# Performance work log

Hardware: AMD Instinct MI355X
Metric: run time of the kernel (lower is better)

Reference implementation:

```python
import jax, jax.numpy as jnp
import numpy as np


def log_g(x):
    # log of the 'continuous' g: g(x) = x + 0.5 for x>=0, sigmoid(x) otherwise
    return jnp.where(x >= 0, jnp.log(jax.nn.relu(x) + 0.5), -jax.nn.softplus(-x))


def setup_inputs() -> dict:
    key = jax.random.key(0)
    ks = jax.random.split(key, 6)
    B, T, D, H = 8, 4096, 1024, 1024
    s = 1.0 / np.sqrt(D)
    return {
        "x": jax.random.normal(ks[0], (B, T, D), dtype=jnp.float32),
        "h_0": jax.random.uniform(ks[1], (B, 1, H), dtype=jnp.float32),
        "Wz": jax.random.normal(ks[2], (D, H), dtype=jnp.float32) * s,
        "bz": jnp.zeros((H,), dtype=jnp.float32),
        "Wh": jax.random.normal(ks[3], (D, H), dtype=jnp.float32) * s,
        "bh": jnp.zeros((H,), dtype=jnp.float32),
    }


def reference(x, h_0, Wz, bz, Wh, bh):
    # x: [B,T,D], h_0: [B,1,H]
    k = jnp.einsum('btd,dh->bth', x, Wz) + bz            # gate pre-activation
    log_z = -jax.nn.softplus(-k)                          # log sigmoid(k)
    log_coeffs = -jax.nn.softplus(k)                      # log (1 - sigmoid(k))
    log_h0 = log_g(h_0)                                   # [B,1,H]
    log_tilde_h = log_g(jnp.einsum('btd,dh->bth', x, Wh) + bh)
    # parallel scan in log space over time axis
    a_star = jnp.pad(jnp.cumsum(log_coeffs, axis=1), ((0, 0), (1, 0), (0, 0)))  # [B,T+1,H]
    log_values = jnp.concatenate([log_h0, log_z + log_tilde_h], axis=1)          # [B,T+1,H]
    log_h = a_star + jax.lax.cumlogsumexp(log_values - a_star, axis=1)
    return jnp.exp(log_h)  # [B,T+1,H]
```

## Files before the change

### kernel.cpp

```cpp
#include <hip/hip_runtime.h>
#include <hip/hip_bf16.h>
#include <cstdint>
#include <cstddef>

#define B_ 8
#define T_ 4096
#define D_ 1024
#define H_ 1024
#define M_ (B_*T_)
#define NCHUNK 64
#define CLEN 64

using bf16x8   = __attribute__((ext_vector_type(8))) __bf16;
using floatx4  = __attribute__((ext_vector_type(4))) float;
using float4v  = __attribute__((ext_vector_type(4))) float;
using ushort4v = __attribute__((ext_vector_type(4))) unsigned short;
using aw2_t    = __attribute__((ext_vector_type(2))) _Float16;
using halfx8   = __attribute__((ext_vector_type(8))) _Float16;

__device__ inline unsigned short f2bf(float f) {
  union { float f; unsigned u; } v; v.f = f;
  unsigned u = v.u;
  u += 0x7fffu + ((u >> 16) & 1u);
  return (unsigned short)(u >> 16);
}

__device__ inline void async_load16(const void* g, void* l) {
  __builtin_amdgcn_global_load_lds((const __attribute__((address_space(1))) void*)g,
                                   (__attribute__((address_space(3))) void*)l,
                                   16, 0, 0);
}

__global__ __launch_bounds__(256) void cast_x_kernel(const float* __restrict__ x,
                                                     unsigned short* __restrict__ xb) {
  size_t i = ((size_t)blockIdx.x * 256 + threadIdx.x) * 2;
#pragma unroll
  for (int j = 0; j < 2; ++j) {
    float4v v = ((const float4v*)x)[i + j];
    ushort4v o = { f2bf(v[0]), f2bf(v[1]), f2bf(v[2]), f2bf(v[3]) };
    ((ushort4v*)xb)[i + j] = o;
  }
}

__global__ __launch_bounds__(256) void transpose_w_kernel(const float* __restrict__ Wz,
                                                          const float* __restrict__ Wh,
                                                          unsigned short* __restrict__ Wzt,
                                                          unsigned short* __restrict__ Wht) {
  __shared__ float tile[32][33];
  const float* W = blockIdx.z ? Wh : Wz;
  unsigned short* Wt = blockIdx.z ? Wht : Wzt;
  int n0 = blockIdx.x * 32, k0 = blockIdx.y * 32;
#pragma unroll
  for (int j = 0; j < 4; ++j) {
    int kr = threadIdx.y + j * 8;
    tile[kr][threadIdx.x] = W[(size_t)(k0 + kr) * H_ + n0 + threadIdx.x];
  }
  __syncthreads();
#pragma unroll
  for (int j = 0; j < 4; ++j) {
    int nr = threadIdx.y + j * 8;
    Wt[(size_t)(n0 + nr) * D_ + k0 + threadIdx.x] = f2bf(tile[threadIdx.x][nr]);
  }
}

__global__ __launch_bounds__(256, 2) void gemm_kernel(
    const unsigned short* __restrict__ xb,
    const unsigned short* __restrict__ wzt,
    const unsigned short* __restrict__ wht,
    const float* __restrict__ bz, const float* __restrict__ bh,
    aw2_t* __restrict__ aw_out) {
  __shared__ __align__(16) unsigned short ldsA[128 * 64];
  __shared__ __align__(16) unsigned short ldsBz[128 * 64];
  __shared__ __align__(16) unsigned short ldsBh[128 * 64];

  const int tid = threadIdx.x;
  const int lane = tid & 63, wid = tid >> 6;
  const int wm = wid >> 1, wn = wid & 1;
  const int row16 = lane & 15, quad = lane >> 4;

  int g = blockIdx.x;
  int x = g & 7, j = g >> 3;
  int n_idx = j & 7;
  int m_idx = (x << 5) | (j >> 3);
  const int m0 = m_idx * 128, n0 = n_idx * 128;

  floatx4 accz[4][4], acch[4][4];
#pragma unroll
  for (int mi = 0; mi < 4; ++mi)
#pragma unroll
    for (int ni = 0; ni < 4; ++ni) {
      accz[mi][ni] = (floatx4){0.f, 0.f, 0.f, 0.f};
      acch[mi][ni] = (floatx4){0.f, 0.f, 0.f, 0.f};
    }

  const int srow = tid >> 3;
  const int jblk = ((tid & 7) - srow) & 7;
  const unsigned short* aSrc  = xb  + (size_t)(m0 + srow) * D_ + jblk * 8;
  const unsigned short* zSrc  = wzt + (size_t)(n0 + srow) * D_ + jblk * 8;
  const unsigned short* hSrc  = wht + (size_t)(n0 + srow) * D_ + jblk * 8;

  const int p0 = (quad + row16) & 7;
  const int p1 = p0 ^ 4;

  for (int kk = 0; kk < D_; kk += 64) {
#pragma unroll
    for (int t = 0; t < 4; ++t) {
      size_t roff = (size_t)(32 * t) * D_ + kk;
      int doff = (tid + 256 * t) * 8;
      async_load16(aSrc + roff, &ldsA[doff]);
      async_load16(zSrc + roff, &ldsBz[doff]);
      async_load16(hSrc + roff, &ldsBh[doff]);
    }
    __syncthreads();

#pragma unroll
    for (int kh = 0; kh < 2; ++kh) {
      const int p = kh ? p1 : p0;
      bf16x8 af[4], bzf[4], bhf[4];
#pragma unroll
      for (int mi = 0; mi < 4; ++mi)
        af[mi] = *(const bf16x8*)&ldsA[(wm * 64 + mi * 16 + row16) * 64 + p * 8];
#pragma unroll
      for (int ni = 0; ni < 4; ++ni) {
        bzf[ni] = *(const bf16x8*)&ldsBz[(wn * 64 + ni * 16 + row16) * 64 + p * 8];
        bhf[ni] = *(const bf16x8*)&ldsBh[(wn * 64 + ni * 16 + row16) * 64 + p * 8];
      }
#pragma unroll
      for (int mi = 0; mi < 4; ++mi)
#pragma unroll
        for (int ni = 0; ni < 4; ++ni) {
          accz[mi][ni] = __builtin_amdgcn_mfma_f32_16x16x32_bf16(af[mi], bzf[ni], accz[mi][ni], 0, 0, 0);
          acch[mi][ni] = __builtin_amdgcn_mfma_f32_16x16x32_bf16(af[mi], bhf[ni], acch[mi][ni], 0, 0, 0);
        }
    }
    __syncthreads();
  }

#pragma unroll
  for (int mi = 0; mi < 4; ++mi) {
#pragma unroll
    for (int ni = 0; ni < 4; ++ni) {
      int col = n0 + wn * 64 + ni * 16 + row16;
      float bzv = bz[col], bhv = bh[col];
#pragma unroll
      for (int r = 0; r < 4; ++r) {
        int row = m0 + wm * 64 + mi * 16 + quad * 4 + r;
        float k   = accz[mi][ni][r] + bzv;
        float pre = acch[mi][ni][r] + bhv;
        float z  = 1.f / (1.f + __expf(-k));
        float av = 1.f / (1.f + __expf(k));
        float gg = (pre >= 0.f) ? (pre + 0.5f) : 1.f / (1.f + __expf(-pre));
        aw2_t o = { (_Float16)av, (_Float16)(z * gg) };
        aw_out[(size_t)row * H_ + col] = o;
      }
    }
  }
}

__global__ __launch_bounds__(256) void scan_pass1(const halfx8* __restrict__ aw,
                                                  float* __restrict__ P, float* __restrict__ S) {
  int c = blockIdx.x;
  int b = blockIdx.y;
  int h4 = threadIdx.x;
  size_t base = (size_t)(b * T_ + c * CLEN) * (H_ / 4) + h4;
  float p0 = 1.f, p1 = 1.f, p2 = 1.f, p3 = 1.f;
  float s0 = 0.f, s1 = 0.f, s2 = 0.f, s3 = 0.f;
#pragma unroll 8
  for (int i = 0; i < CLEN; ++i) {
    halfx8 v = aw[base + (size_t)i * (H_ / 4)];
    float a0 = (float)v[0], w0 = (float)v[1];
    float a1 = (float)v[2], w1 = (float)v[3];
    float a2 = (float)v[4], w2 = (float)v[5];
    float a3 = (float)v[6], w3 = (float)v[7];
    s0 = a0 * s0 + w0; p0 *= a0;
    s1 = a1 * s1 + w1; p1 *= a1;
    s2 = a2 * s2 + w2; p2 *= a2;
    s3 = a3 * s3 + w3; p3 *= a3;
  }
  size_t o = ((size_t)b * H_ + h4 * 4) * NCHUNK + c;
  P[o] = p0; P[o + NCHUNK] = p1; P[o + 2 * NCHUNK] = p2; P[o + 3 * NCHUNK] = p3;
  S[o] = s0; S[o + NCHUNK] = s1; S[o + 2 * NCHUNK] = s2; S[o + 3 * NCHUNK] = s3;
}

__global__ __launch_bounds__(256) void scan_pass2(const float* __restrict__ h0,
                                                  const float* __restrict__ P,
                                                  const float* __restrict__ S,
                                                  float* __restrict__ carry,
                                                  float* __restrict__ out) {
  int gid = blockIdx.x * 256 + threadIdx.x;
  int b = gid >> 10, h = gid & 1023;
  float v = h0[(size_t)b * H_ + h];
  float cur = (v >= 0.f) ? (v + 0.5f) : 1.f / (1.f + __expf(-v));
  out[((size_t)b * (T_ + 1)) * H_ + h] = cur;
  const float4v* Pv = (const float4v*)&P[((size_t)b * H_ + h) * NCHUNK];
  const float4v* Sv = (const float4v*)&S[((size_t)b * H_ + h) * NCHUNK];
  float4v* Cv = (float4v*)&carry[((size_t)b * H_ + h) * NCHUNK];
#pragma unroll
  for (int j = 0; j < NCHUNK / 4; ++j) {
    float4v p = Pv[j], s = Sv[j], cc;
    cc[0] = cur; cur = p[0] * cur + s[0];
    cc[1] = cur; cur = p[1] * cur + s[1];
    cc[2] = cur; cur = p[2] * cur + s[2];
    cc[3] = cur; cur = p[3] * cur + s[3];
    Cv[j] = cc;
  }
}

__global__ __launch_bounds__(256) void scan_pass3(const halfx8* __restrict__ aw,
                                                  const float* __restrict__ carry,
                                                  float* __restrict__ out) {
  int c = blockIdx.x;
  int b = blockIdx.y;
  int h4 = threadIdx.x;
  size_t base = (size_t)(b * T_ + c * CLEN) * (H_ / 4) + h4;
  size_t cb = ((size_t)b * H_ + h4 * 4) * NCHUNK + c;
  float c0 = carry[cb], c1 = carry[cb + NCHUNK], c2 = carry[cb + 2 * NCHUNK], c3 = carry[cb + 3 * NCHUNK];
  size_t obase = ((size_t)b * (T_ + 1) + c * CLEN + 1) * (H_ / 4) + h4;
  float4v* outv = (float4v*)out;
#pragma unroll 8
  for (int i = 0; i < CLEN; ++i) {
    halfx8 v = aw[base + (size_t)i * (H_ / 4)];
    c0 = (float)v[0] * c0 + (float)v[1];
    c1 = (float)v[2] * c1 + (float)v[3];
    c2 = (float)v[4] * c2 + (float)v[5];
    c3 = (float)v[6] * c3 + (float)v[7];
    float4v o = { c0, c1, c2, c3 };
    outv[obase + (size_t)i * (H_ / 4)] = o;
  }
}

extern "C" void kernel_launch(void* const* d_in, const int* in_sizes, int n_in,
                              void* d_out, int out_size, void* d_ws, size_t ws_size,
                              hipStream_t stream) {
  const float* x  = (const float*)d_in[0];
  const float* h0 = (const float*)d_in[1];
  const float* Wz = (const float*)d_in[2];
  const float* bz = (const float*)d_in[3];
  const float* Wh = (const float*)d_in[4];
  const float* bh = (const float*)d_in[5];
  float* out = (float*)d_out;

  char* ws = (char*)d_ws;
  unsigned short* xb  = (unsigned short*)(ws);
  unsigned short* wzt = (unsigned short*)(ws + 67108864ULL);
  unsigned short* wht = (unsigned short*)(ws + 69206016ULL);
  aw2_t* aw_ws = (aw2_t*)(ws + 71303168ULL);
  float* P_ws  = (float*)(ws + 71303168ULL + 134217728ULL);
  float* S_ws  = (float*)(ws + 71303168ULL + 134217728ULL + 2097152ULL);
  float* c_ws  = (float*)(ws + 71303168ULL + 134217728ULL + 2ULL * 2097152ULL);

  hipLaunchKernelGGL(cast_x_kernel, dim3(16384), dim3(256), 0, stream, x, xb);
  hipLaunchKernelGGL(transpose_w_kernel, dim3(32, 32, 2), dim3(32, 8), 0, stream, Wz, Wh, wzt, wht);
  hipLaunchKernelGGL(gemm_kernel, dim3(2048), dim3(256), 0, stream,
                     xb, wzt, wht, bz, bh, aw_ws);
  hipLaunchKernelGGL(scan_pass1, dim3(NCHUNK, B_), dim3(256), 0, stream,
                     (const halfx8*)aw_ws, P_ws, S_ws);
  hipLaunchKernelGGL(scan_pass2, dim3(32), dim3(256), 0, stream, h0, P_ws, S_ws, c_ws, out);
  hipLaunchKernelGGL(scan_pass3, dim3(NCHUNK, B_), dim3(256), 0, stream,
                     (const halfx8*)aw_ws, c_ws, out);
}
```

Baseline: 475.9 us.

## Restructure fused GEMM into 512-thread 256x128 tiles with 4-stage async pipeline

```diff
diff --git a/kernel.cpp b/kernel.cpp
--- a/kernel.cpp
+++ b/kernel.cpp
@@ -63,15 +63,15 @@
   }
 }
 
-__global__ __launch_bounds__(256, 2) void gemm_kernel(
+__global__ __launch_bounds__(512, 2) void gemm_kernel(
     const unsigned short* __restrict__ xb,
     const unsigned short* __restrict__ wzt,
     const unsigned short* __restrict__ wht,
     const float* __restrict__ bz, const float* __restrict__ bh,
     aw2_t* __restrict__ aw_out) {
-  __shared__ __align__(16) unsigned short ldsA[128 * 64];
-  __shared__ __align__(16) unsigned short ldsBz[128 * 64];
-  __shared__ __align__(16) unsigned short ldsBh[128 * 64];
+  __shared__ __align__(16) unsigned short ldsA[4][8192];
+  __shared__ __align__(16) unsigned short ldsBz[4][4096];
+  __shared__ __align__(16) unsigned short ldsBh[4][4096];
 
   const int tid = threadIdx.x;
   const int lane = tid & 63, wid = tid >> 6;
@@ -81,8 +81,8 @@
   int g = blockIdx.x;
   int x = g & 7, j = g >> 3;
   int n_idx = j & 7;
-  int m_idx = (x << 5) | (j >> 3);
-  const int m0 = m_idx * 128, n0 = n_idx * 128;
+  int m_idx = (x << 4) | (j >> 3);
+  const int m0 = m_idx << 8, n0 = n_idx << 7;
 
   floatx4 accz[4][4], acch[4][4];
 #pragma unroll
@@ -93,48 +93,105 @@
       acch[mi][ni] = (floatx4){0.f, 0.f, 0.f, 0.f};
     }
 
-  const int srow = tid >> 3;
-  const int jblk = ((tid & 7) - srow) & 7;
-  const unsigned short* aSrc  = xb  + (size_t)(m0 + srow) * D_ + jblk * 8;
-  const unsigned short* zSrc  = wzt + (size_t)(n0 + srow) * D_ + jblk * 8;
-  const unsigned short* hSrc  = wht + (size_t)(n0 + srow) * D_ + jblk * 8;
-
-  const int p0 = (quad + row16) & 7;
-  const int p1 = p0 ^ 4;
-
-  for (int kk = 0; kk < D_; kk += 64) {
-#pragma unroll
-    for (int t = 0; t < 4; ++t) {
-      size_t roff = (size_t)(32 * t) * D_ + kk;
-      int doff = (tid + 256 * t) * 8;
-      async_load16(aSrc + roff, &ldsA[doff]);
-      async_load16(zSrc + roff, &ldsBz[doff]);
-      async_load16(hSrc + roff, &ldsBh[doff]);
-    }
-    __syncthreads();
-
-#pragma unroll
-    for (int kh = 0; kh < 2; ++kh) {
-      const int p = kh ? p1 : p0;
-      bf16x8 af[4], bzf[4], bhf[4];
-#pragma unroll
-      for (int mi = 0; mi < 4; ++mi)
-        af[mi] = *(const bf16x8*)&ldsA[(wm * 64 + mi * 16 + row16) * 64 + p * 8];
-#pragma unroll
-      for (int ni = 0; ni < 4; ++ni) {
-        bzf[ni] = *(const bf16x8*)&ldsBz[(wn * 64 + ni * 16 + row16) * 64 + p * 8];
-        bhf[ni] = *(const bf16x8*)&ldsBh[(wn * 64 + ni * 16 + row16) * 64 + p * 8];
-      }
-#pragma unroll
-      for (int mi = 0; mi < 4; ++mi)
-#pragma unroll
-        for (int ni = 0; ni < 4; ++ni) {
-          accz[mi][ni] = __builtin_amdgcn_mfma_f32_16x16x32_bf16(af[mi], bzf[ni], accz[mi][ni], 0, 0, 0);
-          acch[mi][ni] = __builtin_amdgcn_mfma_f32_16x16x32_bf16(af[mi], bhf[ni], acch[mi][ni], 0, 0, 0);
-        }
-    }
-    __syncthreads();
-  }
+  const int srow = tid >> 2;
+  const int jA = ((tid & 3) - ((tid >> 3) & 3)) & 3;
+  const unsigned short* aS0 = xb  + (size_t)(m0 + srow) * D_ + jA * 8;
+  const unsigned short* aS1 = aS0 + (size_t)128 * D_;
+  const unsigned short* zS  = wzt + (size_t)(n0 + srow) * D_ + jA * 8;
+  const unsigned short* hS  = wht + (size_t)(n0 + srow) * D_ + jA * 8;
+
+  const int sl = (quad + (row16 >> 1)) & 3;
+  const int aoff = (wm * 64 + row16) * 32 + sl * 8;
+  const int boff = (wn * 64 + row16) * 32 + sl * 8;
+
+  async_load16(aS0 +  0, &ldsA[0][tid * 8]);
+  async_load16(aS1 +  0, &ldsA[0][tid * 8 + 4096]);
+  async_load16(zS  +  0, &ldsBz[0][tid * 8]);
+  async_load16(hS  +  0, &ldsBh[0][tid * 8]);
+  async_load16(aS0 + 32, &ldsA[1][tid * 8]);
+  async_load16(aS1 + 32, &ldsA[1][tid * 8 + 4096]);
+  async_load16(zS  + 32, &ldsBz[1][tid * 8]);
+  async_load16(hS  + 32, &ldsBh[1][tid * 8]);
+  asm volatile("s_waitcnt vmcnt(4)" ::: "memory");
+  __builtin_amdgcn_s_barrier();
+
+#define MFMA16(ACC, BF)                                                          \
+  __builtin_amdgcn_s_setprio(1);                                                 \
+  _Pragma("unroll")                                                              \
+  for (int mi = 0; mi < 4; ++mi)                                                 \
+    _Pragma("unroll")                                                            \
+    for (int ni = 0; ni < 4; ++ni)                                               \
+      ACC[mi][ni] = __builtin_amdgcn_mfma_f32_16x16x32_bf16(af[mi], BF[ni],      \
+                                                            ACC[mi][ni], 0, 0, 0); \
+  __builtin_amdgcn_s_setprio(0);
+
+#pragma unroll 1
+  for (int kt = 0; kt < 16; ++kt) {
+    const int s0 = (2 * kt) & 3, s1 = s0 + 1;
+    const int t0 = (s0 + 2) & 3, t1 = (s0 + 3) & 3;
+    const int kN = ((kt + 1) & 15) * 64;
+    const bool st = (kt < 15);
+    bf16x8 af[4], bzf[4], bhf[4];
+
+#pragma unroll
+    for (int mi = 0; mi < 4; ++mi)
+      af[mi] = *(const bf16x8*)&ldsA[s0][aoff + mi * 512];
+#pragma unroll
+    for (int ni = 0; ni < 4; ++ni)
+      bzf[ni] = *(const bf16x8*)&ldsBz[s0][boff + ni * 512];
+    if (st) {
+      async_load16(aS0 + kN, &ldsA[t0][tid * 8]);
+      async_load16(aS1 + kN, &ldsA[t0][tid * 8 + 4096]);
+    }
+    __builtin_amdgcn_s_barrier();
+    asm volatile("s_waitcnt lgkmcnt(0)" ::: "memory");
+    MFMA16(accz, bzf)
+    __builtin_amdgcn_s_barrier();
+
+#pragma unroll
+    for (int ni = 0; ni < 4; ++ni)
+      bhf[ni] = *(const bf16x8*)&ldsBh[s0][boff + ni * 512];
+    if (st) {
+      async_load16(zS + kN, &ldsBz[t0][tid * 8]);
+      async_load16(hS + kN, &ldsBh[t0][tid * 8]);
+      asm volatile("s_waitcnt vmcnt(4)" ::: "memory");
+    } else {
+      asm volatile("s_waitcnt vmcnt(0)" ::: "memory");
+    }
+    __builtin_amdgcn_s_barrier();
+    asm volatile("s_waitcnt lgkmcnt(0)" ::: "memory");
+    MFMA16(acch, bhf)
+    __builtin_amdgcn_s_barrier();
+
+#pragma unroll
+    for (int mi = 0; mi < 4; ++mi)
+      af[mi] = *(const bf16x8*)&ldsA[s1][aoff + mi * 512];
+#pragma unroll
+    for (int ni = 0; ni < 4; ++ni)
+      bzf[ni] = *(const bf16x8*)&ldsBz[s1][boff + ni * 512];
+    if (st) {
+      async_load16(aS0 + kN + 32, &ldsA[t1][tid * 8]);
+      async_load16(aS1 + kN + 32, &ldsA[t1][tid * 8 + 4096]);
+    }
+    __builtin_amdgcn_s_barrier();
+    asm volatile("s_waitcnt lgkmcnt(0)" ::: "memory");
+    MFMA16(accz, bzf)
+    __builtin_amdgcn_s_barrier();
+
+#pragma unroll
+    for (int ni = 0; ni < 4; ++ni)
+      bhf[ni] = *(const bf16x8*)&ldsBh[s1][boff + ni * 512];
+    if (st) {
+      async_load16(zS + kN + 32, &ldsBz[t1][tid * 8]);
+      async_load16(hS + kN + 32, &ldsBh[t1][tid * 8]);
+      asm volatile("s_waitcnt vmcnt(4)" ::: "memory");
+    }
+    __builtin_amdgcn_s_barrier();
+    asm volatile("s_waitcnt lgkmcnt(0)" ::: "memory");
+    MFMA16(acch, bhf)
+    __builtin_amdgcn_s_barrier();
+  }
+#undef MFMA16
 
 #pragma unroll
   for (int mi = 0; mi < 4; ++mi) {
@@ -251,7 +308,7 @@
 
   hipLaunchKernelGGL(cast_x_kernel, dim3(16384), dim3(256), 0, stream, x, xb);
   hipLaunchKernelGGL(transpose_w_kernel, dim3(32, 32, 2), dim3(32, 8), 0, stream, Wz, Wh, wzt, wht);
-  hipLaunchKernelGGL(gemm_kernel, dim3(2048), dim3(256), 0, stream,
+  hipLaunchKernelGGL(gemm_kernel, dim3(1024), dim3(512), 0, stream,
                      xb, wzt, wht, bz, bh, aw_ws);
   hipLaunchKernelGGL(scan_pass1, dim3(NCHUNK, B_), dim3(256), 0, stream,
                      (const halfx8*)aw_ws, P_ws, S_ws);
```

Measured after the change: 490.9 us. +3.2%, slower.

## Fuse three-pass chunked scan into single decoupled-lookback kernel and merge prep kernels

Applied to the files above, without the earlier changes.

```diff
diff --git a/kernel.cpp b/kernel.cpp
--- a/kernel.cpp
+++ b/kernel.cpp
@@ -31,35 +31,42 @@
                                    16, 0, 0);
 }
 
-__global__ __launch_bounds__(256) void cast_x_kernel(const float* __restrict__ x,
-                                                     unsigned short* __restrict__ xb) {
-  size_t i = ((size_t)blockIdx.x * 256 + threadIdx.x) * 2;
-#pragma unroll
-  for (int j = 0; j < 2; ++j) {
-    float4v v = ((const float4v*)x)[i + j];
-    ushort4v o = { f2bf(v[0]), f2bf(v[1]), f2bf(v[2]), f2bf(v[3]) };
-    ((ushort4v*)xb)[i + j] = o;
-  }
-}
-
-__global__ __launch_bounds__(256) void transpose_w_kernel(const float* __restrict__ Wz,
-                                                          const float* __restrict__ Wh,
-                                                          unsigned short* __restrict__ Wzt,
-                                                          unsigned short* __restrict__ Wht) {
+__global__ __launch_bounds__(256) void prep_kernel(const float* __restrict__ x,
+                                                   unsigned short* __restrict__ xb,
+                                                   const float* __restrict__ Wz,
+                                                   const float* __restrict__ Wh,
+                                                   unsigned short* __restrict__ Wzt,
+                                                   unsigned short* __restrict__ Wht) {
   __shared__ float tile[32][33];
-  const float* W = blockIdx.z ? Wh : Wz;
-  unsigned short* Wt = blockIdx.z ? Wht : Wzt;
-  int n0 = blockIdx.x * 32, k0 = blockIdx.y * 32;
-#pragma unroll
-  for (int j = 0; j < 4; ++j) {
-    int kr = threadIdx.y + j * 8;
-    tile[kr][threadIdx.x] = W[(size_t)(k0 + kr) * H_ + n0 + threadIdx.x];
-  }
-  __syncthreads();
-#pragma unroll
-  for (int j = 0; j < 4; ++j) {
-    int nr = threadIdx.y + j * 8;
-    Wt[(size_t)(n0 + nr) * D_ + k0 + threadIdx.x] = f2bf(tile[threadIdx.x][nr]);
+  const int bid = blockIdx.x;
+  if (bid < 16384) {
+    size_t i = ((size_t)bid * 256 + threadIdx.x) * 2;
+#pragma unroll
+    for (int j = 0; j < 2; ++j) {
+      float4v v = ((const float4v*)x)[i + j];
+      ushort4v o = { f2bf(v[0]), f2bf(v[1]), f2bf(v[2]), f2bf(v[3]) };
+      ((ushort4v*)xb)[i + j] = o;
+    }
+  } else {
+    const int b2 = bid - 16384;
+    const int z = b2 >> 10;
+    const int rem = b2 & 1023;
+    const int bx = rem & 31, by = rem >> 5;
+    const int tx = threadIdx.x & 31, ty = threadIdx.x >> 5;
+    const float* W = z ? Wh : Wz;
+    unsigned short* Wt = z ? Wht : Wzt;
+    const int n0 = bx * 32, k0 = by * 32;
+#pragma unroll
+    for (int j = 0; j < 4; ++j) {
+      int kr = ty + j * 8;
+      tile[kr][tx] = W[(size_t)(k0 + kr) * H_ + n0 + tx];
+    }
+    __syncthreads();
+#pragma unroll
+    for (int j = 0; j < 4; ++j) {
+      int nr = ty + j * 8;
+      Wt[(size_t)(n0 + nr) * D_ + k0 + tx] = f2bf(tile[tx][nr]);
+    }
   }
 }
 
@@ -157,12 +164,18 @@
   }
 }
 
-__global__ __launch_bounds__(256) void scan_pass1(const halfx8* __restrict__ aw,
-                                                  float* __restrict__ P, float* __restrict__ S) {
-  int c = blockIdx.x;
-  int b = blockIdx.y;
-  int h4 = threadIdx.x;
-  size_t base = (size_t)(b * T_ + c * CLEN) * (H_ / 4) + h4;
+__global__ __launch_bounds__(256) void scan_fused(const halfx8* __restrict__ aw,
+                                                  const float* __restrict__ h0,
+                                                  float4v* __restrict__ PL,
+                                                  float4v* __restrict__ SL,
+                                                  float4v* __restrict__ SI,
+                                                  int* __restrict__ flags,
+                                                  float* __restrict__ out) {
+  const int c = blockIdx.x & (NCHUNK - 1);
+  const int b = blockIdx.x >> 6;
+  const int h4 = threadIdx.x;
+  const size_t base = (size_t)(b * T_ + c * CLEN) * (H_ / 4) + h4;
+
   float p0 = 1.f, p1 = 1.f, p2 = 1.f, p3 = 1.f;
   float s0 = 0.f, s1 = 0.f, s2 = 0.f, s3 = 0.f;
 #pragma unroll 8
@@ -177,46 +190,65 @@
     s2 = a2 * s2 + w2; p2 *= a2;
     s3 = a3 * s3 + w3; p3 *= a3;
   }
-  size_t o = ((size_t)b * H_ + h4 * 4) * NCHUNK + c;
-  P[o] = p0; P[o + NCHUNK] = p1; P[o + 2 * NCHUNK] = p2; P[o + 3 * NCHUNK] = p3;
-  S[o] = s0; S[o + NCHUNK] = s1; S[o + 2 * NCHUNK] = s2; S[o + 3 * NCHUNK] = s3;
-}
-
-__global__ __launch_bounds__(256) void scan_pass2(const float* __restrict__ h0,
-                                                  const float* __restrict__ P,
-                                                  const float* __restrict__ S,
-                                                  float* __restrict__ carry,
-                                                  float* __restrict__ out) {
-  int gid = blockIdx.x * 256 + threadIdx.x;
-  int b = gid >> 10, h = gid & 1023;
-  float v = h0[(size_t)b * H_ + h];
-  float cur = (v >= 0.f) ? (v + 0.5f) : 1.f / (1.f + __expf(-v));
-  out[((size_t)b * (T_ + 1)) * H_ + h] = cur;
-  const float4v* Pv = (const float4v*)&P[((size_t)b * H_ + h) * NCHUNK];
-  const float4v* Sv = (const float4v*)&S[((size_t)b * H_ + h) * NCHUNK];
-  float4v* Cv = (float4v*)&carry[((size_t)b * H_ + h) * NCHUNK];
-#pragma unroll
-  for (int j = 0; j < NCHUNK / 4; ++j) {
-    float4v p = Pv[j], s = Sv[j], cc;
-    cc[0] = cur; cur = p[0] * cur + s[0];
-    cc[1] = cur; cur = p[1] * cur + s[1];
-    cc[2] = cur; cur = p[2] * cur + s[2];
-    cc[3] = cur; cur = p[3] * cur + s[3];
-    Cv[j] = cc;
-  }
-}
-
-__global__ __launch_bounds__(256) void scan_pass3(const halfx8* __restrict__ aw,
-                                                  const float* __restrict__ carry,
-                                                  float* __restrict__ out) {
-  int c = blockIdx.x;
-  int b = blockIdx.y;
-  int h4 = threadIdx.x;
-  size_t base = (size_t)(b * T_ + c * CLEN) * (H_ / 4) + h4;
-  size_t cb = ((size_t)b * H_ + h4 * 4) * NCHUNK + c;
-  float c0 = carry[cb], c1 = carry[cb + NCHUNK], c2 = carry[cb + 2 * NCHUNK], c3 = carry[cb + 3 * NCHUNK];
-  size_t obase = ((size_t)b * (T_ + 1) + c * CLEN + 1) * (H_ / 4) + h4;
+  const size_t pidx = (size_t)(b * NCHUNK + c) * 256 + h4;
+  PL[pidx] = (float4v){p0, p1, p2, p3};
+  SL[pidx] = (float4v){s0, s1, s2, s3};
+  __threadfence();
+  __syncthreads();
+  if (threadIdx.x == 0)
+    __hip_atomic_store(&flags[b * NCHUNK + c], 1, __ATOMIC_RELEASE, __HIP_MEMORY_SCOPE_AGENT);
+
+  __shared__ int sflag;
+  float4v Pr = (float4v){1.f, 1.f, 1.f, 1.f};
+  float4v Sr = (float4v){0.f, 0.f, 0.f, 0.f};
+  float4v Hin;
+  int idx = c - 1;
+  for (;;) {
+    if (idx < 0) {
+      const float4v hv = *(const float4v*)&h0[(size_t)b * H_ + h4 * 4];
+      float4v g;
+#pragma unroll
+      for (int j = 0; j < 4; ++j)
+        g[j] = (hv[j] >= 0.f) ? (hv[j] + 0.5f) : 1.f / (1.f + __expf(-hv[j]));
+      Hin = Pr * g + Sr;
+      break;
+    }
+    if (threadIdx.x == 0) {
+      int f = __hip_atomic_load(&flags[b * NCHUNK + idx], __ATOMIC_ACQUIRE, __HIP_MEMORY_SCOPE_AGENT);
+      while (f == 0) {
+        __builtin_amdgcn_s_sleep(2);
+        f = __hip_atomic_load(&flags[b * NCHUNK + idx], __ATOMIC_ACQUIRE, __HIP_MEMORY_SCOPE_AGENT);
+      }
+      sflag = f;
+    }
+    __syncthreads();
+    const int f = sflag;
+    __syncthreads();
+    const size_t q = (size_t)(b * NCHUNK + idx) * 256 + h4;
+    if (f == 2) { Hin = Pr * SI[q] + Sr; break; }
+    Sr = Pr * SL[q] + Sr;
+    Pr = Pr * PL[q];
+    --idx;
+  }
+
+  SI[pidx] = (float4v){p0 * Hin[0] + s0, p1 * Hin[1] + s1, p2 * Hin[2] + s2, p3 * Hin[3] + s3};
+  __threadfence();
+  __syncthreads();
+  if (threadIdx.x == 0)
+    __hip_atomic_store(&flags[b * NCHUNK + c], 2, __ATOMIC_RELEASE, __HIP_MEMORY_SCOPE_AGENT);
+
   float4v* outv = (float4v*)out;
+  if (c == 0) {
+    const float4v hv = *(const float4v*)&h0[(size_t)b * H_ + h4 * 4];
+    float4v g;
+#pragma unroll
+    for (int j = 0; j < 4; ++j)
+      g[j] = (hv[j] >= 0.f) ? (hv[j] + 0.5f) : 1.f / (1.f + __expf(-hv[j]));
+    outv[(size_t)b * (T_ + 1) * (H_ / 4) + h4] = g;
+  }
+
+  float c0 = Hin[0], c1 = Hin[1], c2 = Hin[2], c3 = Hin[3];
+  const size_t obase = ((size_t)b * (T_ + 1) + c * CLEN + 1) * (H_ / 4) + h4;
 #pragma unroll 8
   for (int i = 0; i < CLEN; ++i) {
     halfx8 v = aw[base + (size_t)i * (H_ / 4)];
@@ -224,8 +256,7 @@
     c1 = (float)v[2] * c1 + (float)v[3];
     c2 = (float)v[4] * c2 + (float)v[5];
     c3 = (float)v[6] * c3 + (float)v[7];
-    float4v o = { c0, c1, c2, c3 };
-    outv[obase + (size_t)i * (H_ / 4)] = o;
+    outv[obase + (size_t)i * (H_ / 4)] = (float4v){c0, c1, c2, c3};
   }
 }
 
@@ -245,17 +276,16 @@
   unsigned short* wzt = (unsigned short*)(ws + 67108864ULL);
   unsigned short* wht = (unsigned short*)(ws + 69206016ULL);
   aw2_t* aw_ws = (aw2_t*)(ws + 71303168ULL);
-  float* P_ws  = (float*)(ws + 71303168ULL + 134217728ULL);
-  float* S_ws  = (float*)(ws + 71303168ULL + 134217728ULL + 2097152ULL);
-  float* c_ws  = (float*)(ws + 71303168ULL + 134217728ULL + 2ULL * 2097152ULL);
-
-  hipLaunchKernelGGL(cast_x_kernel, dim3(16384), dim3(256), 0, stream, x, xb);
-  hipLaunchKernelGGL(transpose_w_kernel, dim3(32, 32, 2), dim3(32, 8), 0, stream, Wz, Wh, wzt, wht);
+  float4v* PL_ws = (float4v*)(ws + 71303168ULL + 134217728ULL);
+  float4v* SL_ws = (float4v*)(ws + 71303168ULL + 134217728ULL + 2097152ULL);
+  float4v* SI_ws = (float4v*)(ws + 71303168ULL + 134217728ULL + 2ULL * 2097152ULL);
+  int* flags = (int*)(ws + 67108864ULL - 2048ULL);
+
+  hipLaunchKernelGGL(prep_kernel, dim3(16384 + 2048), dim3(256), 0, stream,
+                     x, xb, Wz, Wh, wzt, wht);
   hipLaunchKernelGGL(gemm_kernel, dim3(2048), dim3(256), 0, stream,
                      xb, wzt, wht, bz, bh, aw_ws);
-  hipLaunchKernelGGL(scan_pass1, dim3(NCHUNK, B_), dim3(256), 0, stream,
-                     (const halfx8*)aw_ws, P_ws, S_ws);
-  hipLaunchKernelGGL(scan_pass2, dim3(32), dim3(256), 0, stream, h0, P_ws, S_ws, c_ws, out);
-  hipLaunchKernelGGL(scan_pass3, dim3(NCHUNK, B_), dim3(256), 0, stream,
-                     (const halfx8*)aw_ws, c_ws, out);
-}
+  hipMemsetAsync(flags, 0, (size_t)(B_ * NCHUNK) * sizeof(int), stream);
+  hipLaunchKernelGGL(scan_fused, dim3(B_ * NCHUNK), dim3(256), 0, stream,
+                     (const halfx8*)aw_ws, h0, PL_ws, SL_ws, SI_ws, flags, out);
+}
```

New measurement: 657.0 us. 38.1% more time.

## Fuse scan chunk reduction into GEMM epilogue and merge prep kernels

Applied to the files above, without the earlier changes.

```diff
diff --git a/kernel.cpp b/kernel.cpp
--- a/kernel.cpp
+++ b/kernel.cpp
@@ -14,8 +14,10 @@
 using bf16x8   = __attribute__((ext_vector_type(8))) __bf16;
 using floatx4  = __attribute__((ext_vector_type(4))) float;
 using float4v  = __attribute__((ext_vector_type(4))) float;
+using float2v  = __attribute__((ext_vector_type(2))) float;
 using ushort4v = __attribute__((ext_vector_type(4))) unsigned short;
 using aw2_t    = __attribute__((ext_vector_type(2))) _Float16;
+using halfx4   = __attribute__((ext_vector_type(4))) _Float16;
 using halfx8   = __attribute__((ext_vector_type(8))) _Float16;
 
 __device__ inline unsigned short f2bf(float f) {
@@ -31,35 +33,42 @@
                                    16, 0, 0);
 }
 
-__global__ __launch_bounds__(256) void cast_x_kernel(const float* __restrict__ x,
-                                                     unsigned short* __restrict__ xb) {
-  size_t i = ((size_t)blockIdx.x * 256 + threadIdx.x) * 2;
-#pragma unroll
-  for (int j = 0; j < 2; ++j) {
-    float4v v = ((const float4v*)x)[i + j];
-    ushort4v o = { f2bf(v[0]), f2bf(v[1]), f2bf(v[2]), f2bf(v[3]) };
-    ((ushort4v*)xb)[i + j] = o;
-  }
-}
-
-__global__ __launch_bounds__(256) void transpose_w_kernel(const float* __restrict__ Wz,
-                                                          const float* __restrict__ Wh,
-                                                          unsigned short* __restrict__ Wzt,
-                                                          unsigned short* __restrict__ Wht) {
+__global__ __launch_bounds__(256) void prep_kernel(const float* __restrict__ x,
+                                                   unsigned short* __restrict__ xb,
+                                                   const float* __restrict__ Wz,
+                                                   const float* __restrict__ Wh,
+                                                   unsigned short* __restrict__ Wzt,
+                                                   unsigned short* __restrict__ Wht) {
   __shared__ float tile[32][33];
-  const float* W = blockIdx.z ? Wh : Wz;
-  unsigned short* Wt = blockIdx.z ? Wht : Wzt;
-  int n0 = blockIdx.x * 32, k0 = blockIdx.y * 32;
-#pragma unroll
-  for (int j = 0; j < 4; ++j) {
-    int kr = threadIdx.y + j * 8;
-    tile[kr][threadIdx.x] = W[(size_t)(k0 + kr) * H_ + n0 + threadIdx.x];
-  }
-  __syncthreads();
-#pragma unroll
-  for (int j = 0; j < 4; ++j) {
-    int nr = threadIdx.y + j * 8;
-    Wt[(size_t)(n0 + nr) * D_ + k0 + threadIdx.x] = f2bf(tile[threadIdx.x][nr]);
+  const int bid = blockIdx.x;
+  if (bid < 16384) {
+    size_t i = ((size_t)bid * 256 + threadIdx.x) * 2;
+#pragma unroll
+    for (int j = 0; j < 2; ++j) {
+      float4v v = ((const float4v*)x)[i + j];
+      ushort4v o = { f2bf(v[0]), f2bf(v[1]), f2bf(v[2]), f2bf(v[3]) };
+      ((ushort4v*)xb)[i + j] = o;
+    }
+  } else {
+    const int b2 = bid - 16384;
+    const int z = b2 >> 10;
+    const int rem = b2 & 1023;
+    const int bx = rem & 31, by = rem >> 5;
+    const int tx = threadIdx.x & 31, ty = threadIdx.x >> 5;
+    const float* W = z ? Wh : Wz;
+    unsigned short* Wt = z ? Wht : Wzt;
+    const int n0 = bx * 32, k0 = by * 32;
+#pragma unroll
+    for (int j = 0; j < 4; ++j) {
+      int kr = ty + j * 8;
+      tile[kr][tx] = W[(size_t)(k0 + kr) * H_ + n0 + tx];
+    }
+    __syncthreads();
+#pragma unroll
+    for (int j = 0; j < 4; ++j) {
+      int nr = ty + j * 8;
+      Wt[(size_t)(n0 + nr) * D_ + k0 + tx] = f2bf(tile[tx][nr]);
+    }
   }
 }
 
@@ -68,7 +77,8 @@
     const unsigned short* __restrict__ wzt,
     const unsigned short* __restrict__ wht,
     const float* __restrict__ bz, const float* __restrict__ bh,
-    aw2_t* __restrict__ aw_out) {
+    aw2_t* __restrict__ aw_out,
+    float* __restrict__ P_ws, float* __restrict__ S_ws) {
   __shared__ __align__(16) unsigned short ldsA[128 * 64];
   __shared__ __align__(16) unsigned short ldsBz[128 * 64];
   __shared__ __align__(16) unsigned short ldsBh[128 * 64];
@@ -136,50 +146,45 @@
     __syncthreads();
   }
 
-#pragma unroll
-  for (int mi = 0; mi < 4; ++mi) {
-#pragma unroll
-    for (int ni = 0; ni < 4; ++ni) {
-      int col = n0 + wn * 64 + ni * 16 + row16;
-      float bzv = bz[col], bhv = bh[col];
+  const int b_of = m0 >> 12;
+  const int cidx = ((m0 & (T_ - 1)) >> 6) + wm;
+#pragma unroll
+  for (int ni = 0; ni < 4; ++ni) {
+    const int col = n0 + wn * 64 + ni * 16 + row16;
+    const float bzv = bz[col], bhv = bh[col];
+    float Pc = 1.f, Sc = 0.f;
+#pragma unroll
+    for (int mi = 0; mi < 4; ++mi) {
+      float pm = 1.f, sm = 0.f;
 #pragma unroll
       for (int r = 0; r < 4; ++r) {
-        int row = m0 + wm * 64 + mi * 16 + quad * 4 + r;
+        const int row = m0 + wm * 64 + mi * 16 + quad * 4 + r;
         float k   = accz[mi][ni][r] + bzv;
         float pre = acch[mi][ni][r] + bhv;
         float z  = 1.f / (1.f + __expf(-k));
         float av = 1.f / (1.f + __expf(k));
         float gg = (pre >= 0.f) ? (pre + 0.5f) : 1.f / (1.f + __expf(-pre));
-        aw2_t o = { (_Float16)av, (_Float16)(z * gg) };
+        _Float16 ah = (_Float16)av, wh = (_Float16)(z * gg);
+        aw2_t o = { ah, wh };
         aw_out[(size_t)row * H_ + col] = o;
+        float afv = (float)ah, wfv = (float)wh;
+        sm = afv * sm + wfv;
+        pm = afv * pm;
       }
-    }
-  }
-}
-
-__global__ __launch_bounds__(256) void scan_pass1(const halfx8* __restrict__ aw,
-                                                  float* __restrict__ P, float* __restrict__ S) {
-  int c = blockIdx.x;
-  int b = blockIdx.y;
-  int h4 = threadIdx.x;
-  size_t base = (size_t)(b * T_ + c * CLEN) * (H_ / 4) + h4;
-  float p0 = 1.f, p1 = 1.f, p2 = 1.f, p3 = 1.f;
-  float s0 = 0.f, s1 = 0.f, s2 = 0.f, s3 = 0.f;
-#pragma unroll 8
-  for (int i = 0; i < CLEN; ++i) {
-    halfx8 v = aw[base + (size_t)i * (H_ / 4)];
-    float a0 = (float)v[0], w0 = (float)v[1];
-    float a1 = (float)v[2], w1 = (float)v[3];
-    float a2 = (float)v[4], w2 = (float)v[5];
-    float a3 = (float)v[6], w3 = (float)v[7];
-    s0 = a0 * s0 + w0; p0 *= a0;
-    s1 = a1 * s1 + w1; p1 *= a1;
-    s2 = a2 * s2 + w2; p2 *= a2;
-    s3 = a3 * s3 + w3; p3 *= a3;
-  }
-  size_t o = ((size_t)b * H_ + h4 * 4) * NCHUNK + c;
-  P[o] = p0; P[o + NCHUNK] = p1; P[o + 2 * NCHUNK] = p2; P[o + 3 * NCHUNK] = p3;
-  S[o] = s0; S[o + NCHUNK] = s1; S[o + 2 * NCHUNK] = s2; S[o + 3 * NCHUNK] = s3;
+      float pp = __shfl_xor(pm, 16), sp = __shfl_xor(sm, 16);
+      sm = (quad & 1) ? (pm * sp + sm) : (pp * sm + sp);
+      pm = pm * pp;
+      pp = __shfl_xor(pm, 32); sp = __shfl_xor(sm, 32);
+      sm = (quad & 2) ? (pm * sp + sm) : (pp * sm + sp);
+      pm = pm * pp;
+      Sc = pm * Sc + sm;
+      Pc = pm * Pc;
+    }
+    if (quad == 0) {
+      size_t o = ((size_t)b_of * H_ + col) * NCHUNK + cidx;
+      P_ws[o] = Pc; S_ws[o] = Sc;
+    }
+  }
 }
 
 __global__ __launch_bounds__(256) void scan_pass2(const float* __restrict__ h0,
@@ -206,26 +211,23 @@
   }
 }
 
-__global__ __launch_bounds__(256) void scan_pass3(const halfx8* __restrict__ aw,
+__global__ __launch_bounds__(512) void scan_pass3(const halfx4* __restrict__ aw,
                                                   const float* __restrict__ carry,
                                                   float* __restrict__ out) {
   int c = blockIdx.x;
   int b = blockIdx.y;
-  int h4 = threadIdx.x;
-  size_t base = (size_t)(b * T_ + c * CLEN) * (H_ / 4) + h4;
-  size_t cb = ((size_t)b * H_ + h4 * 4) * NCHUNK + c;
-  float c0 = carry[cb], c1 = carry[cb + NCHUNK], c2 = carry[cb + 2 * NCHUNK], c3 = carry[cb + 3 * NCHUNK];
-  size_t obase = ((size_t)b * (T_ + 1) + c * CLEN + 1) * (H_ / 4) + h4;
-  float4v* outv = (float4v*)out;
+  int h2 = threadIdx.x;
+  size_t base = (size_t)(b * T_ + c * CLEN) * (H_ / 2) + h2;
+  size_t cb = ((size_t)b * H_ + h2 * 2) * NCHUNK + c;
+  float c0 = carry[cb], c1 = carry[cb + NCHUNK];
+  size_t obase = ((size_t)b * (T_ + 1) + c * CLEN + 1) * (H_ / 2) + h2;
+  float2v* outv = (float2v*)out;
 #pragma unroll 8
   for (int i = 0; i < CLEN; ++i) {
-    halfx8 v = aw[base + (size_t)i * (H_ / 4)];
+    halfx4 v = aw[base + (size_t)i * (H_ / 2)];
     c0 = (float)v[0] * c0 + (float)v[1];
     c1 = (float)v[2] * c1 + (float)v[3];
-    c2 = (float)v[4] * c2 + (float)v[5];
-    c3 = (float)v[6] * c3 + (float)v[7];
-    float4v o = { c0, c1, c2, c3 };
-    outv[obase + (size_t)i * (H_ / 4)] = o;
+    outv[obase + (size_t)i * (H_ / 2)] = (float2v){c0, c1};
   }
 }
 
@@ -249,13 +251,11 @@
   float* S_ws  = (float*)(ws + 71303168ULL + 134217728ULL + 2097152ULL);
   float* c_ws  = (float*)(ws + 71303168ULL + 134217728ULL + 2ULL * 2097152ULL);
 
-  hipLaunchKernelGGL(cast_x_kernel, dim3(16384), dim3(256), 0, stream, x, xb);
-  hipLaunchKernelGGL(transpose_w_kernel, dim3(32, 32, 2), dim3(32, 8), 0, stream, Wz, Wh, wzt, wht);
+  hipLaunchKernelGGL(prep_kernel, dim3(16384 + 2048), dim3(256), 0, stream,
+                     x, xb, Wz, Wh, wzt, wht);
   hipLaunchKernelGGL(gemm_kernel, dim3(2048), dim3(256), 0, stream,
-                     xb, wzt, wht, bz, bh, aw_ws);
-  hipLaunchKernelGGL(scan_pass1, dim3(NCHUNK, B_), dim3(256), 0, stream,
-                     (const halfx8*)aw_ws, P_ws, S_ws);
+                     xb, wzt, wht, bz, bh, aw_ws, P_ws, S_ws);
   hipLaunchKernelGGL(scan_pass2, dim3(32), dim3(256), 0, stream, h0, P_ws, S_ws, c_ws, out);
-  hipLaunchKernelGGL(scan_pass3, dim3(NCHUNK, B_), dim3(256), 0, stream,
-                     (const halfx8*)aw_ws, c_ws, out);
-}
+  hipLaunchKernelGGL(scan_pass3, dim3(NCHUNK, B_), dim3(512), 0, stream,
+                     (const halfx4*)aw_ws, c_ws, out);
+}
```

Result: faster. 462.6 us (-2.8%).
